# Kernel tuning notes

Hardware: AMD Instinct MI355X
Metric: run time of the kernel (lower is better)

The kernel has to match this reference:

```python
import jax, jax.numpy as jnp
import numpy as np

N, E, G = 50000, 640000, 256
NODE_IN, EDGE_IN, H, L, T = 64, 16, 128, 4, 5
BN_EPS = 1e-5

def setup_inputs() -> dict:
    key = jax.random.key(0)
    ks = jax.random.split(key, 24)
    s = lambda k, shape, fan: jax.random.normal(k, shape, jnp.float32) * (1.0 / np.sqrt(fan))
    return {
        "x": jax.random.normal(ks[0], (N, NODE_IN), jnp.float32),
        "edge_attr": jax.random.normal(ks[1], (E, EDGE_IN), jnp.float32),
        "node_w": s(ks[2], (NODE_IN, H), NODE_IN), "node_b": jnp.zeros((H,), jnp.float32),
        "edge_w1": s(ks[3], (EDGE_IN, H), EDGE_IN), "edge_b1": jnp.zeros((H,), jnp.float32),
        "edge_w2": s(ks[4], (H, H), H), "edge_b2": jnp.zeros((H,), jnp.float32),
        "conv_w1": s(ks[5], (L, H, H), H), "conv_b1": jnp.zeros((L, H), jnp.float32),
        "conv_w2": s(ks[6], (L, H, H), H), "conv_b2": jnp.zeros((L, H), jnp.float32),
        "bn_gamma": jnp.ones((L, H), jnp.float32), "bn_beta": jnp.zeros((L, H), jnp.float32),
        "gate_w1": s(ks[7], (H, H // 2), H), "gate_b1": jnp.zeros((H // 2,), jnp.float32),
        "gate_w2": s(ks[8], (H // 2, 1), H // 2), "gate_b2": jnp.zeros((1,), jnp.float32),
        "head_w1": s(ks[9], (H, H), H), "head_b1": jnp.zeros((H,), jnp.float32),
        "head_w2": s(ks[10], (H, T), H), "head_b2": jnp.zeros((T,), jnp.float32),
        "edge_index": jax.random.randint(ks[11], (2, E), 0, N, jnp.int32),
        "batch": jnp.sort(jax.random.randint(ks[12], (N,), 0, G, jnp.int32)),
    }

def reference(x, edge_attr, node_w, node_b, edge_w1, edge_b1, edge_w2, edge_b2,
              conv_w1, conv_b1, conv_w2, conv_b2, bn_gamma, bn_beta,
              gate_w1, gate_b1, gate_w2, gate_b2, head_w1, head_b1, head_w2, head_b2,
              edge_index, batch):
    relu = jax.nn.relu
    h = x @ node_w + node_b                                   # [N,H]
    e = relu(edge_attr @ edge_w1 + edge_b1) @ edge_w2 + edge_b2  # [E,H]
    src, dst = edge_index[0], edge_index[1]
    bn_scale = 1.0 / jnp.sqrt(jnp.float32(1.0) + BN_EPS)      # eval BN: mean=0, var=1
    for l in range(L):
        m = relu(h[src] + e)                                  # GINEConv message [E,H]
        aggr = jax.ops.segment_sum(m, dst, num_segments=N)    # scatter-add
        z = h + aggr                                          # eps=0: (1+eps)*x + aggr
        z = relu(z @ conv_w1[l] + conv_b1[l]) @ conv_w2[l] + conv_b2[l]
        z = z * bn_scale * bn_gamma[l] + bn_beta[l]
        h = relu(z)                                           # dropout off (eval)
    gate = relu(h @ gate_w1 + gate_b1) @ gate_w2 + gate_b2    # [N,1]
    gmax = jax.ops.segment_max(gate, batch, num_segments=G)   # segment softmax
    wexp = jnp.exp(gate - gmax[batch])
    denom = jax.ops.segment_sum(wexp, batch, num_segments=G)
    alpha = wexp / denom[batch]
    g = jax.ops.segment_sum(alpha * h, batch, num_segments=G) # [G,H]
    return relu(g @ head_w1 + head_b1) @ head_w2 + head_b2    # [G,T]
```

## Files before the change

kernel.cpp:

```cpp
#include <hip/hip_runtime.h>

typedef unsigned short u16;
typedef __bf16 bf16x8 __attribute__((ext_vector_type(8)));
typedef __bf16 bf16x2 __attribute__((ext_vector_type(2)));
typedef float f32x4 __attribute__((ext_vector_type(4)));
typedef unsigned short u16x8 __attribute__((ext_vector_type(8)));

#define NNODES 50000
#define NEDGES 640000
#define NGRAPH 256
#define HCHUNK 4096
#define HSPLIT 64
#define NCHUNK 13

__device__ __forceinline__ float bf2f(u16 u) {
  unsigned int v = ((unsigned int)u) << 16; float f; __builtin_memcpy(&f, &v, 4); return f;
}
__device__ __forceinline__ u16 f2bf(float f) {
  unsigned int x; __builtin_memcpy(&x, &f, 4);
  unsigned int lsb = (x >> 16) & 1u;
  x += 0x7fffu + lsb;
  return (u16)(x >> 16);
}
__device__ __forceinline__ unsigned int pkbf(float a, float b) {
  bf16x2 p; p[0] = (__bf16)a; p[1] = (__bf16)b;
  unsigned int r; __builtin_memcpy(&r, &p, 4); return r;
}

__global__ void write_zero_f32(float* __restrict__ out, int n) {
  int i = blockIdx.x * 256 + threadIdx.x;
  if (i < n) out[i] = 0.f;
}

__global__ void prep_weights(const float* __restrict__ node_w, const float* __restrict__ edge_w1,
                             const float* __restrict__ edge_w2, const float* __restrict__ conv_w1,
                             const float* __restrict__ conv_w2, const float* __restrict__ gate_w1,
                             u16* __restrict__ node_wt, u16* __restrict__ edge_w1t,
                             u16* __restrict__ edge_w2t, u16* __restrict__ conv_w1t,
                             u16* __restrict__ conv_w2t, u16* __restrict__ gate_w1t) {
  int o = blockIdx.x * 256 + threadIdx.x;
  if (o < 8192) { int n = o >> 6, k = o & 63; node_wt[o] = f2bf(node_w[k * 128 + n]); return; }
  o -= 8192;
  if (o < 4096) { int n = o >> 5, k = o & 31;
                  edge_w1t[o] = (k < 16) ? f2bf(edge_w1[k * 128 + n]) : (u16)0; return; }
  o -= 4096;
  if (o < 16384) { int n = o >> 7, k = o & 127; edge_w2t[o] = f2bf(edge_w2[k * 128 + n]); return; }
  o -= 16384;
  if (o < 65536) { int l = o >> 14, r = o & 16383, n = r >> 7, k = r & 127;
                   conv_w1t[o] = f2bf(conv_w1[l * 16384 + k * 128 + n]); return; }
  o -= 65536;
  if (o < 65536) { int l = o >> 14, r = o & 16383, n = r >> 7, k = r & 127;
                   conv_w2t[o] = f2bf(conv_w2[l * 16384 + k * 128 + n]); return; }
  o -= 65536;
  if (o < 8192) { int n = o >> 7, k = o & 127; gate_w1t[o] = f2bf(gate_w1[k * 64 + n]); }
}

__global__ __launch_bounds__(256) void hist_k(const int* __restrict__ dst,
                                              int* __restrict__ partial) {
  __shared__ int hloc[HCHUNK];
  int b = blockIdx.x, t = threadIdx.x;
  int c = b >> 6, sp = b & 63;
  for (int j = t; j < HCHUNK; j += 256) hloc[j] = 0;
  __syncthreads();
  int base = c * HCHUNK;
  int e0 = sp * (NEDGES / HSPLIT), e1 = e0 + NEDGES / HSPLIT;
  for (int i = e0 + t; i < e1; i += 256) {
    int d = dst[i] - base;
    if ((unsigned)d < HCHUNK) atomicAdd(&hloc[d], 1);
  }
  __syncthreads();
  for (int j = t; j < HCHUNK; j += 256) {
    int g = base + j;
    if (g < NNODES) partial[(size_t)sp * NNODES + g] = hloc[j];
  }
}
__global__ __launch_bounds__(256) void scan_a(int* __restrict__ partial,
                                              int* __restrict__ counts,
                                              int* __restrict__ bsums,
                                              const int* __restrict__ batch,
                                              int* __restrict__ goffs, int n) {
  __shared__ int sh4[4];
  int b = blockIdx.x, t = threadIdx.x;
  int lane = t & 63, w = t >> 6;
  if (b == 196) {
    int lo = 0, hi = n;
    while (lo < hi) { int mid = (lo + hi) >> 1; if (batch[mid] < t) lo = mid + 1; else hi = mid; }
    goffs[t] = lo;
    if (t == 0) goffs[256] = n;
    return;
  }
  int g = b * 256 + t;
  int run = 0;
  if (g < n) {
    for (int sp = 0; sp < HSPLIT; sp++) {
      int v = partial[(size_t)sp * NNODES + g];
      partial[(size_t)sp * NNODES + g] = run;
      run += v;
    }
    counts[g] = run;
  }
  int s = run;
  for (int mm = 32; mm; mm >>= 1) s += __shfl_xor(s, mm, 64);
  if (lane == 0) sh4[w] = s;
  __syncthreads();
  if (t == 0) bsums[b] = sh4[0] + sh4[1] + sh4[2] + sh4[3];
}
__global__ __launch_bounds__(256) void scan_c(const int* __restrict__ counts,
                                              const int* __restrict__ bsums,
                                              int* __restrict__ offs, int n) {
  __shared__ int sh4[4];
  __shared__ int wt_[4];
  __shared__ int base_sh;
  int b = blockIdx.x, t = threadIdx.x;
  int lane = t & 63, w = t >> 6;
  int v = (t < b) ? bsums[t] : 0;
  int sv = v;
  for (int mm = 32; mm; mm >>= 1) sv += __shfl_xor(sv, mm, 64);
  if (lane == 0) sh4[w] = sv;
  __syncthreads();
  if (t == 0) base_sh = sh4[0] + sh4[1] + sh4[2] + sh4[3];
  int g = b * 256 + t;
  int x = (g < n) ? counts[g] : 0;
  int inc = x;
  for (int d = 1; d < 64; d <<= 1) { int y = __shfl_up(inc, (unsigned)d, 64); if (lane >= d) inc += y; }
  if (lane == 63) wt_[w] = inc;
  __syncthreads();
  int add = base_sh;
  for (int i = 0; i < w; i++) add += wt_[i];
  int excl = add + inc - x;
  if (g < n) offs[g] = excl;
  if (b == 0 && t == 0) offs[n] = NEDGES;
}
__global__ __launch_bounds__(256) void scatter_k(const int* __restrict__ src,
                                                 const int* __restrict__ dst,
                                                 const int* __restrict__ offs,
                                                 const int* __restrict__ partial,
                                                 int* __restrict__ csr_src,
                                                 int* __restrict__ inv) {
  __shared__ int hloc[HCHUNK];
  int b = blockIdx.x, t = threadIdx.x;
  int c = b >> 6, sp = b & 63;
  for (int j = t; j < HCHUNK; j += 256) hloc[j] = 0;
  __syncthreads();
  int base = c * HCHUNK;
  int e0 = sp * (NEDGES / HSPLIT), e1 = e0 + NEDGES / HSPLIT;
  for (int i = e0 + t; i < e1; i += 256) {
    int d = dst[i];
    int dl = d - base;
    if ((unsigned)dl < HCHUNK) {
      int r = atomicAdd(&hloc[dl], 1);
      int p = offs[d] + partial[(size_t)sp * NNODES + d] + r;
      csr_src[p] = src[i];
      inv[i] = p;
    }
  }
}

template <int KB, int SA, int SB>
__device__ __forceinline__ void mfma_block(const u16* aL, const u16* bL, int m, int quad,
                                           int rbase, f32x4* acc) {
#pragma unroll
  for (int kb = 0; kb < KB; ++kb) {
    bf16x8 a = *(const bf16x8*)(aL + (rbase + m) * SA + kb * 32 + quad * 8);
#pragma unroll
    for (int nt = 0; nt < 8; ++nt) {
      bf16x8 b = *(const bf16x8*)(bL + (nt * 16 + m) * SB + kb * 32 + quad * 8);
      acc[nt] = __builtin_amdgcn_mfma_f32_16x16x32_bf16(a, b, acc[nt], 0, 0, 0);
    }
  }
}

__global__ __launch_bounds__(256) void node_encode(const float* __restrict__ x,
                                                   const u16* __restrict__ wt,
                                                   const float* __restrict__ nb,
                                                   u16* __restrict__ hb, int n) {
  __shared__ alignas(16) u16 sA[64 * 72];
  __shared__ alignas(16) u16 sW[128 * 72];
  int t = threadIdx.x;
  int row0 = blockIdx.x * 64;
#pragma unroll
  for (int i = 0; i < 4; i++) {
    int idx = t + 256 * i; int r = idx >> 4, c = idx & 15;
    int grow = row0 + r; if (grow > n - 1) grow = n - 1;
    float4 v = *(const float4*)(x + (size_t)grow * 64 + c * 4);
    ushort4 o; o.x = f2bf(v.x); o.y = f2bf(v.y); o.z = f2bf(v.z); o.w = f2bf(v.w);
    *(ushort4*)&sA[r * 72 + c * 4] = o;
  }
#pragma unroll
  for (int i = 0; i < 4; i++) {
    int idx = t + 256 * i; int nr = idx >> 3, c = idx & 7;
    *(uint4*)&sW[nr * 72 + c * 8] = *(const uint4*)(wt + nr * 64 + c * 8);
  }
  __syncthreads();
  int lane = t & 63, w = t >> 6, m = lane & 15, quad = lane >> 4, rbase = w * 16;
  f32x4 acc[8];
  f32x4 z4 = {0.f, 0.f, 0.f, 0.f};
#pragma unroll
  for (int i = 0; i < 8; i++) acc[i] = z4;
  mfma_block<2, 72, 72>(sA, sW, m, quad, rbase, acc);
#pragma unroll
  for (int nt = 0; nt < 8; nt++) {
    int col = nt * 16 + m;
    float bb = nb[col];
    f32x4 a4 = acc[nt];
#pragma unroll
    for (int r = 0; r < 4; r++) {
      int grow = row0 + rbase + quad * 4 + r;
      if (grow < n) hb[(size_t)grow * 128 + col] = f2bf(a4[r] + bb);
    }
  }
}

__global__ __launch_bounds__(256) void edge_encode(const float* __restrict__ ea,
                                                   const u16* __restrict__ w1t,
                                                   const u16* __restrict__ w2t,
                                                   const float* __restrict__ b1,
                                                   const float* __restrict__ b2,
                                                   const int* __restrict__ inv,
                                                   u16* __restrict__ e_perm) {
  __shared__ alignas(16) u16 sMid[128 * 132];
  int t = threadIdx.x;
  int lane = t & 63, w = t >> 6, m = lane & 15, quad = lane >> 4;
  int s0 = blockIdx.x * 128;
  int ebase = w * 32;

  bf16x8 af[2];
#pragma unroll
  for (int rt2 = 0; rt2 < 2; rt2++) {
    int eid = s0 + ebase + rt2 * 16 + m;
    bf16x8 a = {};
    if (quad < 2) {
      float4 v0 = *(const float4*)(ea + (size_t)eid * 16 + quad * 8);
      float4 v1 = *(const float4*)(ea + (size_t)eid * 16 + quad * 8 + 4);
      a[0] = (__bf16)v0.x; a[1] = (__bf16)v0.y; a[2] = (__bf16)v0.z; a[3] = (__bf16)v0.w;
      a[4] = (__bf16)v1.x; a[5] = (__bf16)v1.y; a[6] = (__bf16)v1.z; a[7] = (__bf16)v1.w;
    }
    af[rt2] = a;
  }
  bf16x8 w1f[8];
#pragma unroll
  for (int nt = 0; nt < 8; nt++)
    w1f[nt] = *(const bf16x8*)(w1t + (nt * 16 + m) * 32 + quad * 8);

  f32x4 z4 = {0.f, 0.f, 0.f, 0.f};
  f32x4 acc1[16];
#pragma unroll
  for (int i = 0; i < 16; i++) acc1[i] = z4;
#pragma unroll
  for (int rt2 = 0; rt2 < 2; rt2++) {
#pragma unroll
    for (int nt = 0; nt < 8; nt++)
      acc1[rt2 * 8 + nt] = __builtin_amdgcn_mfma_f32_16x16x32_bf16(w1f[nt], af[rt2], acc1[rt2 * 8 + nt], 0, 0, 0);
  }
#pragma unroll
  for (int rt2 = 0; rt2 < 2; rt2++) {
#pragma unroll
    for (int nt = 0; nt < 8; nt++) {
      float4 bb = *(const float4*)&b1[nt * 16 + quad * 4];
      f32x4 a4 = acc1[rt2 * 8 + nt];
      uint2 pk;
      pk.x = pkbf(fmaxf(a4[0] + bb.x, 0.f), fmaxf(a4[1] + bb.y, 0.f));
      pk.y = pkbf(fmaxf(a4[2] + bb.z, 0.f), fmaxf(a4[3] + bb.w, 0.f));
      *(uint2*)&sMid[(ebase + rt2 * 16 + m) * 132 + nt * 16 + quad * 4] = pk;
    }
  }
  bf16x8 w2f[8];
  float4 b2v[2];
#pragma unroll
  for (int ct = 0; ct < 2; ct++) {
    b2v[ct] = *(const float4*)&b2[w * 32 + ct * 16 + quad * 4];
#pragma unroll
    for (int kb = 0; kb < 4; kb++)
      w2f[ct * 4 + kb] = *(const bf16x8*)(w2t + (size_t)(w * 32 + ct * 16 + m) * 128 + kb * 32 + quad * 8);
  }
  __syncthreads();

  f32x4 acc2[16];
#pragma unroll
  for (int i = 0; i < 16; i++) acc2[i] = z4;
#pragma unroll
  for (int rt = 0; rt < 8; rt++) {
#pragma unroll
    for (int kb = 0; kb < 4; kb++) {
      bf16x8 a = *(const bf16x8*)(&sMid[(rt * 16 + m) * 132 + kb * 32 + quad * 8]);
      acc2[rt * 2 + 0] = __builtin_amdgcn_mfma_f32_16x16x32_bf16(w2f[kb], a, acc2[rt * 2 + 0], 0, 0, 0);
      acc2[rt * 2 + 1] = __builtin_amdgcn_mfma_f32_16x16x32_bf16(w2f[4 + kb], a, acc2[rt * 2 + 1], 0, 0, 0);
    }
  }
  __syncthreads();
#pragma unroll
  for (int rt = 0; rt < 8; rt++) {
#pragma unroll
    for (int ct = 0; ct < 2; ct++) {
      f32x4 a4 = acc2[rt * 2 + ct];
      uint2 pk;
      pk.x = pkbf(a4[0] + b2v[ct].x, a4[1] + b2v[ct].y);
      pk.y = pkbf(a4[2] + b2v[ct].z, a4[3] + b2v[ct].w);
      *(uint2*)&sMid[(rt * 16 + m) * 132 + w * 32 + ct * 16 + quad * 4] = pk;
    }
  }
  __syncthreads();
#pragma unroll
  for (int i = 0; i < 8; i++) {
    int idx = t + 256 * i; int r = idx >> 4, c = idx & 15;
    int R = inv[s0 + r];
    *(uint4*)(e_perm + (size_t)R * 128 + c * 8) = *(const uint4*)&sMid[r * 132 + c * 8];
  }
}

template <bool GATE>
__global__ __launch_bounds__(256) void layer_k(const u16* __restrict__ hin,
                                               u16* __restrict__ hout,
                                               const u16* __restrict__ e_perm,
                                               const int* __restrict__ offs,
                                               const int* __restrict__ csr_src,
                                               const u16* __restrict__ w1t, const u16* __restrict__ w2t,
                                               const float* __restrict__ b1, const float* __restrict__ b2,
                                               const float* __restrict__ gam, const float* __restrict__ bet,
                                               const u16* __restrict__ gw1t, const float* __restrict__ gb1,
                                               const float* __restrict__ gw2, const float* __restrict__ gb2,
                                               float* __restrict__ gate_out, int n) {
  __shared__ alignas(16) u16 sZ[64 * 132];
  __shared__ alignas(16) u16 sMid[64 * 132];
  int t = threadIdx.x;
  int lane = t & 63, w = t >> 6, m = lane & 15, quad = lane >> 4;
  int row0 = blockIdx.x * 64;
  int li = m;

  int oidx = row0 + w * 16 + (lane < 16 ? lane : 16);
  if (oidx > n) oidx = n;
  int offv = offs[oidx];

  for (int k = 0; k < 4; k++) {
    int lr = w * 16 + quad * 4 + k;
    int nd = row0 + lr;
    int ndc = (nd > n - 1) ? (n - 1) : nd;
    int e0 = __shfl(offv, quad * 4 + k, 64), e1 = __shfl(offv, quad * 4 + k + 1, 64);
    u16x8 hv = *(const u16x8*)(hin + (size_t)ndc * 128 + li * 8);
    float a[8];
#pragma unroll
    for (int j = 0; j < 8; j++) a[j] = 0.f;
    int s = e0;
    for (; s + 2 <= e1; s += 2) {
      int v0 = csr_src[s], v1 = csr_src[s + 1];
      u16x8 h0 = *(const u16x8*)(hin + (size_t)v0 * 128 + li * 8);
      u16x8 ee0 = *(const u16x8*)(e_perm + (size_t)s * 128 + li * 8);
      u16x8 h1 = *(const u16x8*)(hin + (size_t)v1 * 128 + li * 8);
      u16x8 ee1 = *(const u16x8*)(e_perm + (size_t)(s + 1) * 128 + li * 8);
#pragma unroll
      for (int j = 0; j < 8; j++) {
        a[j] += fmaxf(bf2f(h0[j]) + bf2f(ee0[j]), 0.f);
        a[j] += fmaxf(bf2f(h1[j]) + bf2f(ee1[j]), 0.f);
      }
    }
    if (s < e1) {
      int v = csr_src[s];
      u16x8 hgv = *(const u16x8*)(hin + (size_t)v * 128 + li * 8);
      u16x8 ev = *(const u16x8*)(e_perm + (size_t)s * 128 + li * 8);
#pragma unroll
      for (int j = 0; j < 8; j++) a[j] += fmaxf(bf2f(hgv[j]) + bf2f(ev[j]), 0.f);
    }
    bf16x8 o;
#pragma unroll
    for (int j = 0; j < 8; j++) o[j] = (__bf16)(bf2f(hv[j]) + a[j]);
    *(bf16x8*)&sZ[lr * 132 + li * 8] = o;
  }
  bf16x8 w1f[8];
  float4 b1v[2];
#pragma unroll
  for (int ct = 0; ct < 2; ct++) {
    b1v[ct] = *(const float4*)&b1[w * 32 + ct * 16 + quad * 4];
#pragma unroll
    for (int kb = 0; kb < 4; kb++)
      w1f[ct * 4 + kb] = *(const bf16x8*)(w1t + (size_t)(w * 32 + ct * 16 + m) * 128 + kb * 32 + quad * 8);
  }
  __syncthreads();

  f32x4 z4 = {0.f, 0.f, 0.f, 0.f};
  f32x4 acc[8];
#pragma unroll
  for (int i = 0; i < 8; i++) acc[i] = z4;
#pragma unroll
  for (int rt = 0; rt < 4; rt++) {
#pragma unroll
    for (int kb = 0; kb < 4; kb++) {
      bf16x8 a = *(const bf16x8*)(&sZ[(rt * 16 + m) * 132 + kb * 32 + quad * 8]);
      acc[rt * 2 + 0] = __builtin_amdgcn_mfma_f32_16x16x32_bf16(w1f[kb], a, acc[rt * 2 + 0], 0, 0, 0);
      acc[rt * 2 + 1] = __builtin_amdgcn_mfma_f32_16x16x32_bf16(w1f[4 + kb], a, acc[rt * 2 + 1], 0, 0, 0);
    }
  }
#pragma unroll
  for (int rt = 0; rt < 4; rt++) {
#pragma unroll
    for (int ct = 0; ct < 2; ct++) {
      f32x4 a4 = acc[rt * 2 + ct];
      uint2 pk;
      pk.x = pkbf(fmaxf(a4[0] + b1v[ct].x, 0.f), fmaxf(a4[1] + b1v[ct].y, 0.f));
      pk.y = pkbf(fmaxf(a4[2] + b1v[ct].z, 0.f), fmaxf(a4[3] + b1v[ct].w, 0.f));
      *(uint2*)&sMid[(rt * 16 + m) * 132 + w * 32 + ct * 16 + quad * 4] = pk;
    }
  }
  bf16x8 w2f[8];
  float4 b2v[2], gamv[2], betv[2];
#pragma unroll
  for (int ct = 0; ct < 2; ct++) {
    int c0 = w * 32 + ct * 16 + quad * 4;
    b2v[ct] = *(const float4*)&b2[c0];
    gamv[ct] = *(const float4*)&gam[c0];
    betv[ct] = *(const float4*)&bet[c0];
#pragma unroll
    for (int kb = 0; kb < 4; kb++)
      w2f[ct * 4 + kb] = *(const bf16x8*)(w2t + (size_t)(w * 32 + ct * 16 + m) * 128 + kb * 32 + quad * 8);
  }
  __syncthreads();

  f32x4 acc2[8];
#pragma unroll
  for (int i = 0; i < 8; i++) acc2[i] = z4;
#pragma unroll
  for (int rt = 0; rt < 4; rt++) {
#pragma unroll
    for (int kb = 0; kb < 4; kb++) {
      bf16x8 a = *(const bf16x8*)(&sMid[(rt * 16 + m) * 132 + kb * 32 + quad * 8]);
      acc2[rt * 2 + 0] = __builtin_amdgcn_mfma_f32_16x16x32_bf16(w2f[kb], a, acc2[rt * 2 + 0], 0, 0, 0);
      acc2[rt * 2 + 1] = __builtin_amdgcn_mfma_f32_16x16x32_bf16(w2f[4 + kb], a, acc2[rt * 2 + 1], 0, 0, 0);
    }
  }
  const float bns = 0.99999500003749983f;
#pragma unroll
  for (int rt = 0; rt < 4; rt++) {
#pragma unroll
    for (int ct = 0; ct < 2; ct++) {
      f32x4 a4 = acc2[rt * 2 + ct];
      uint2 pk;
      pk.x = pkbf(fmaxf((a4[0] + b2v[ct].x) * bns * gamv[ct].x + betv[ct].x, 0.f),
                  fmaxf((a4[1] + b2v[ct].y) * bns * gamv[ct].y + betv[ct].y, 0.f));
      pk.y = pkbf(fmaxf((a4[2] + b2v[ct].z) * bns * gamv[ct].z + betv[ct].z, 0.f),
                  fmaxf((a4[3] + b2v[ct].w) * bns * gamv[ct].w + betv[ct].w, 0.f));
      *(uint2*)&sZ[(rt * 16 + m) * 132 + w * 32 + ct * 16 + quad * 4] = pk;
    }
  }
  __syncthreads();
#pragma unroll
  for (int i = 0; i < 4; i++) {
    int idx = t + 256 * i; int r = idx >> 4, c = idx & 15;
    int grow = row0 + r;
    if (grow < n)
      *(uint4*)(hout + (size_t)grow * 128 + c * 8) = *(const uint4*)&sZ[r * 132 + c * 8];
  }

  if (GATE) {
    int rbase = w * 16;
    f32x4 gacc[4];
#pragma unroll
    for (int i = 0; i < 4; i++) gacc[i] = z4;
#pragma unroll
    for (int kb = 0; kb < 4; kb++) {
      bf16x8 a = *(const bf16x8*)(&sZ[(rbase + m) * 132 + kb * 32 + quad * 8]);
#pragma unroll
      for (int nt = 0; nt < 4; nt++) {
        bf16x8 b = *(const bf16x8*)(gw1t + (nt * 16 + m) * 128 + kb * 32 + quad * 8);
        gacc[nt] = __builtin_amdgcn_mfma_f32_16x16x32_bf16(a, b, gacc[nt], 0, 0, 0);
      }
    }
    float gb1v[4], gw2v[4];
#pragma unroll
    for (int nt = 0; nt < 4; nt++) { gb1v[nt] = gb1[nt * 16 + m]; gw2v[nt] = gw2[nt * 16 + m]; }
    float gb2v = gb2[0];
#pragma unroll
    for (int r = 0; r < 4; r++) {
      float p = 0.f;
#pragma unroll
      for (int nt = 0; nt < 4; nt++) p += fmaxf(gacc[nt][r] + gb1v[nt], 0.f) * gw2v[nt];
      p += __shfl_xor(p, 1, 64);
      p += __shfl_xor(p, 2, 64);
      p += __shfl_xor(p, 4, 64);
      p += __shfl_xor(p, 8, 64);
      if (m == 0) {
        int grow = row0 + rbase + quad * 4 + r;
        if (grow < n) gate_out[grow] = p + gb2v;
      }
    }
  }
}

__global__ __launch_bounds__(256) void pool_head_k(const float* __restrict__ gate,
                                                   const u16* __restrict__ hb,
                                                   const int* __restrict__ goffs,
                                                   const float* __restrict__ hw1,
                                                   const float* __restrict__ hb1,
                                                   const float* __restrict__ hw2,
                                                   const float* __restrict__ hb2,
                                                   float* __restrict__ out) {
  int g = blockIdx.x, t = threadIdx.x;
  int s0 = goffs[g], s1 = goffs[g + 1];
  int lane = t & 63, w = t >> 6;
  __shared__ float red[4];
  __shared__ float fin[2][128];
  __shared__ float shid[128];
  float mx = -3.4e38f;
  for (int i = s0 + t; i < s1; i += 256) mx = fmaxf(mx, gate[i]);
  for (int d = 32; d; d >>= 1) mx = fmaxf(mx, __shfl_xor(mx, d, 64));
  if (lane == 0) red[w] = mx;
  __syncthreads();
  mx = fmaxf(fmaxf(red[0], red[1]), fmaxf(red[2], red[3]));
  __syncthreads();
  float sm = 0.f;
  for (int i = s0 + t; i < s1; i += 256) sm += __expf(gate[i] - mx);
  for (int d = 32; d; d >>= 1) sm += __shfl_xor(sm, d, 64);
  if (lane == 0) red[w] = sm;
  __syncthreads();
  sm = red[0] + red[1] + red[2] + red[3];
  int g2 = t >> 7, tc = t & 127;
  float acc = 0.f;
  for (int i = s0 + g2; i < s1; i += 2)
    acc += __expf(gate[i] - mx) * bf2f(hb[(size_t)i * 128 + tc]);
  fin[g2][tc] = acc;
  __syncthreads();
  if (t < 128) fin[0][t] = (s1 > s0) ? (fin[0][t] + fin[1][t]) / sm : 0.f;
  __syncthreads();
  if (t < 128) {
    float s = 0.f;
    for (int k = 0; k < 128; k++) s += fin[0][k] * hw1[k * 128 + t];
    shid[t] = fmaxf(s + hb1[t], 0.f);
  }
  __syncthreads();
  if (t < 5) {
    float o = hb2[t];
    for (int k = 0; k < 128; k++) o += shid[k] * hw2[k * 5 + t];
    out[g * 5 + t] = o;
  }
}

extern "C" void kernel_launch(void* const* d_in, const int* in_sizes, int n_in,
                              void* d_out, int out_size, void* d_ws, size_t ws_size,
                              hipStream_t stream) {
  const int N = NNODES, E = NEDGES, G = NGRAPH;
  const float* x = (const float*)d_in[0];
  const float* edge_attr = (const float*)d_in[1];
  const float* node_w = (const float*)d_in[2];
  const float* node_b = (const float*)d_in[3];
  const float* edge_w1 = (const float*)d_in[4];
  const float* edge_b1 = (const float*)d_in[5];
  const float* edge_w2 = (const float*)d_in[6];
  const float* edge_b2 = (const float*)d_in[7];
  const float* conv_w1 = (const float*)d_in[8];
  const float* conv_b1 = (const float*)d_in[9];
  const float* conv_w2 = (const float*)d_in[10];
  const float* conv_b2 = (const float*)d_in[11];
  const float* bn_gamma = (const float*)d_in[12];
  const float* bn_beta = (const float*)d_in[13];
  const float* gate_w1 = (const float*)d_in[14];
  const float* gate_b1 = (const float*)d_in[15];
  const float* gate_w2 = (const float*)d_in[16];
  const float* gate_b2 = (const float*)d_in[17];
  const float* head_w1 = (const float*)d_in[18];
  const float* head_b1 = (const float*)d_in[19];
  const float* head_w2 = (const float*)d_in[20];
  const float* head_b2 = (const float*)d_in[21];
  const int* eidx = (const int*)d_in[22];
  const int* batch = (const int*)d_in[23];
  const int* esrc = eidx;
  const int* edst = eidx + E;

  char* wp = (char*)d_ws;
  auto alloc = [&](size_t bytes) { char* p = wp; wp += (bytes + 255) & ~(size_t)255; return p; };
  u16* e_perm = (u16*)alloc((size_t)E * 128 * 2);
  u16* hb = (u16*)alloc((size_t)(N + 16) * 128 * 2);
  u16* hb2 = (u16*)alloc((size_t)(N + 16) * 128 * 2);
  float* gate = (float*)alloc((size_t)N * 4);
  int* counts = (int*)alloc((size_t)N * 4);
  int* offs = (int*)alloc((size_t)(N + 1) * 4);
  int* partial = (int*)alloc((size_t)HSPLIT * N * 4);
  int* csr_src = (int*)alloc((size_t)E * 4);
  int* inv = (int*)alloc((size_t)E * 4);
  int* bsums = (int*)alloc(256 * 4);
  int* goffs = (int*)alloc((G + 1) * 4);
  u16* node_wt = (u16*)alloc(8192 * 2);
  u16* edge_w1t = (u16*)alloc(4096 * 2);
  u16* edge_w2t = (u16*)alloc(16384 * 2);
  u16* conv_w1t = (u16*)alloc(65536 * 2);
  u16* conv_w2t = (u16*)alloc(65536 * 2);
  u16* gate_w1t = (u16*)alloc(8192 * 2);

  size_t need = (size_t)(wp - (char*)d_ws);
  if (need > ws_size) {
    write_zero_f32<<<(out_size + 255) / 256, 256, 0, stream>>>((float*)d_out, out_size);
    return;
  }

  prep_weights<<<656, 256, 0, stream>>>(node_w, edge_w1, edge_w2, conv_w1, conv_w2, gate_w1,
                                        node_wt, edge_w1t, edge_w2t, conv_w1t, conv_w2t, gate_w1t);
  hist_k<<<NCHUNK * HSPLIT, 256, 0, stream>>>(edst, partial);
  scan_a<<<197, 256, 0, stream>>>(partial, counts, bsums, batch, goffs, N);
  scan_c<<<196, 256, 0, stream>>>(counts, bsums, offs, N);
  scatter_k<<<NCHUNK * HSPLIT, 256, 0, stream>>>(esrc, edst, offs, partial, csr_src, inv);
  node_encode<<<(N + 63) / 64, 256, 0, stream>>>(x, node_wt, node_b, hb, N);
  edge_encode<<<E / 128, 256, 0, stream>>>(edge_attr, edge_w1t, edge_w2t, edge_b1, edge_b2,
                                           inv, e_perm);
  u16* hcur = hb;
  u16* hnext = hb2;
  for (int l = 0; l < 4; l++) {
    if (l < 3)
      layer_k<false><<<(N + 63) / 64, 256, 0, stream>>>(hcur, hnext, e_perm, offs, csr_src,
                                                        conv_w1t + l * 16384, conv_w2t + l * 16384,
                                                        conv_b1 + l * 128, conv_b2 + l * 128,
                                                        bn_gamma + l * 128, bn_beta + l * 128,
                                                        gate_w1t, gate_b1, gate_w2, gate_b2,
                                                        (float*)nullptr, N);
    else
      layer_k<true><<<(N + 63) / 64, 256, 0, stream>>>(hcur, hnext, e_perm, offs, csr_src,
                                                       conv_w1t + l * 16384, conv_w2t + l * 16384,
                                                       conv_b1 + l * 128, conv_b2 + l * 128,
                                                       bn_gamma + l * 128, bn_beta + l * 128,
                                                       gate_w1t, gate_b1, gate_w2, gate_b2,
                                                       gate, N);
    u16* tmp = hcur; hcur = hnext; hnext = tmp;
  }
  pool_head_k<<<G, 256, 0, stream>>>(gate, hcur, goffs, head_w1, head_b1, head_w2, head_b2,
                                     (float*)d_out);
}
```

Baseline: 554.4 us.

## Balance edge aggregation across quad groups by edge count instead of node count

The gather-aggregate phase of the layer kernel used to give each 16-lane quad group a fixed four destination nodes. It now stages the block's 65 CSR offsets in shared memory and splits the block's edge range into 16 equal chunks. Each quad group binary-searches for its first node and handles every node whose edge range starts inside its chunk. The goal is to even out per-group work when node degrees vary, at the cost of an extra __syncthreads, a small binary search and a variable number of nodes per group, which adds divergence within a wave.

Result: slower. 576.1 us (+3.9%).

```diff
diff --git a/kernel.cpp b/kernel.cpp
--- a/kernel.cpp
+++ b/kernel.cpp
@@ -322,26 +322,42 @@
                                                float* __restrict__ gate_out, int n) {
   __shared__ alignas(16) u16 sZ[64 * 132];
   __shared__ alignas(16) u16 sMid[64 * 132];
+  __shared__ int sOffs[65];
   int t = threadIdx.x;
   int lane = t & 63, w = t >> 6, m = lane & 15, quad = lane >> 4;
   int row0 = blockIdx.x * 64;
   int li = m;
 
-  int oidx = row0 + w * 16 + (lane < 16 ? lane : 16);
-  if (oidx > n) oidx = n;
-  int offv = offs[oidx];
-
-  for (int k = 0; k < 4; k++) {
-    int lr = w * 16 + quad * 4 + k;
-    int nd = row0 + lr;
+  if (t < 65) {
+    int bl = row0 + t; if (bl > n) bl = n;
+    sOffs[t] = offs[bl];
+  }
+  __syncthreads();
+
+  int e0b = sOffs[0], e1b = sOffs[64];
+  int tot = e1b - e0b;
+  int chunk = (tot + 15) >> 4; if (chunk < 1) chunk = 1;
+  int qq = w * 4 + quad;
+  int tgt = e0b + qq * chunk;
+  int tgtend = tgt + chunk;
+
+  int lo_l = 0, hi_l = 64;
+  while (lo_l < hi_l) {
+    int mid = (lo_l + hi_l) >> 1;
+    if (sOffs[mid] < tgt) lo_l = mid + 1; else hi_l = mid;
+  }
+  for (int l = lo_l; l < 64; l++) {
+    int ev0 = sOffs[l];
+    if (qq < 15 && ev0 >= tgtend) break;
+    int ev1 = sOffs[l + 1];
+    int nd = row0 + l;
     int ndc = (nd > n - 1) ? (n - 1) : nd;
-    int e0 = __shfl(offv, quad * 4 + k, 64), e1 = __shfl(offv, quad * 4 + k + 1, 64);
     u16x8 hv = *(const u16x8*)(hin + (size_t)ndc * 128 + li * 8);
     float a[8];
 #pragma unroll
     for (int j = 0; j < 8; j++) a[j] = 0.f;
-    int s = e0;
-    for (; s + 2 <= e1; s += 2) {
+    int s = ev0;
+    for (; s + 2 <= ev1; s += 2) {
       int v0 = csr_src[s], v1 = csr_src[s + 1];
       u16x8 h0 = *(const u16x8*)(hin + (size_t)v0 * 128 + li * 8);
       u16x8 ee0 = *(const u16x8*)(e_perm + (size_t)s * 128 + li * 8);
@@ -353,7 +369,7 @@
         a[j] += fmaxf(bf2f(h1[j]) + bf2f(ee1[j]), 0.f);
       }
     }
-    if (s < e1) {
+    if (s < ev1) {
       int v = csr_src[s];
       u16x8 hgv = *(const u16x8*)(hin + (size_t)v * 128 + li * 8);
       u16x8 ev = *(const u16x8*)(e_perm + (size_t)s * 128 + li * 8);
@@ -363,7 +379,7 @@
     bf16x8 o;
 #pragma unroll
     for (int j = 0; j < 8; j++) o[j] = (__bf16)(bf2f(hv[j]) + a[j]);
-    *(bf16x8*)&sZ[lr * 132 + li * 8] = o;
+    *(bf16x8*)&sZ[l * 132 + li * 8] = o;
   }
   bf16x8 w1f[8];
   float4 b1v[2];
```
